# Optimization experiments

Hardware: AMD Instinct MI355X
Metric: run time of the kernel (lower is better)

## Reference

```python
import jax, jax.numpy as jnp
import numpy as np

POLY_Q = 2.0  # normalizer='poly_2'
N_HEADS = 12
LN_EPS = 1e-5  # torch nn.LayerNorm default


def poly_norm(x, q=POLY_Q):
    # Newton solve for c such that sum_k 1/(-x-c)^q == 1, row-wise (last axis).
    c = jnp.min(-x, axis=-1, keepdims=True) - 1.0  # ensures -x - c >= 1
    for _ in range(6):
        base = -x - c
        poly_sum = jnp.sum(base ** (-q), axis=-1, keepdims=True)
        poly_sum_der = q * jnp.sum(base ** (-(q + 1.0)), axis=-1, keepdims=True)
        c = c - (poly_sum - 1.0) / (poly_sum_der + 1e-8)
    return (-x - c) ** (-q)


def layer_norm(x, g, b, eps=LN_EPS):
    m = jnp.mean(x, axis=-1, keepdims=True)
    v = jnp.mean((x - m) ** 2, axis=-1, keepdims=True)
    return (x - m) * jax.lax.rsqrt(v + eps) * g + b


def setup_inputs() -> dict:
    key = jax.random.key(0)
    B, S, D, M = 2, 1024, 768, 3072
    ks = jax.random.split(key, 8)
    sd = 1.0 / np.sqrt(D)
    sm = 1.0 / np.sqrt(M)
    return {
        "x": jax.random.normal(ks[0], (B, S, D), dtype=jnp.float32),
        "ln1_g": jnp.ones((D,), jnp.float32),
        "ln1_b": jnp.zeros((D,), jnp.float32),
        "wq": jax.random.normal(ks[1], (D, D), jnp.float32) * sd,
        "bq": jnp.zeros((D,), jnp.float32),
        "wk": jax.random.normal(ks[2], (D, D), jnp.float32) * sd,
        "bk": jnp.zeros((D,), jnp.float32),
        "wv": jax.random.normal(ks[3], (D, D), jnp.float32) * sd,
        "bv": jnp.zeros((D,), jnp.float32),
        "wo": jax.random.normal(ks[4], (D, D), jnp.float32) * sd,
        "bo": jnp.zeros((D,), jnp.float32),
        "ln2_g": jnp.ones((D,), jnp.float32),
        "ln2_b": jnp.zeros((D,), jnp.float32),
        "w1": jax.random.normal(ks[5], (D, M), jnp.float32) * sd,
        "b1": jnp.zeros((M,), jnp.float32),
        "w2": jax.random.normal(ks[6], (M, D), jnp.float32) * sm,
        "b2": jnp.zeros((D,), jnp.float32),
    }


def reference(x, ln1_g, ln1_b, wq, bq, wk, bk, wv, bv, wo, bo,
              ln2_g, ln2_b, w1, b1, w2, b2):
    B, S, D = x.shape
    H = N_HEADS
    Dh = D // H
    # --- pre-LN self-attention with poly normalizer ---
    y = layer_norm(x, ln1_g, ln1_b)
    q = (y @ wq + bq).reshape(B, S, H, Dh) / jnp.sqrt(jnp.float32(Dh))
    k = (y @ wk + bk).reshape(B, S, H, Dh)
    v = (y @ wv + bv).reshape(B, S, H, Dh)
    scores = jnp.einsum('bqhd,bkhd->bhqk', q, k)  # [B,H,S,S]
    attn_w = poly_norm(scores)
    attn = jnp.einsum('bhqk,bkhd->bqhd', attn_w, v).reshape(B, S, D)
    x1 = x + attn @ wo + bo  # residual 1
    # --- MLP block ---
    y2 = layer_norm(x1, ln2_g, ln2_b)
    h = jax.nn.gelu(y2 @ w1 + b1, approximate=False)  # torch GELU = exact erf
    out = x1 + h @ w2 + b2  # residual 2
    return out
```

## Files before the change

### kernel.cpp

```cpp
#include <hip/hip_runtime.h>

#define DEV __device__ __forceinline__

typedef unsigned short u16;
typedef __attribute__((ext_vector_type(8))) short bf16x8;
typedef __attribute__((ext_vector_type(4))) float f32x4;
typedef __attribute__((ext_vector_type(4))) unsigned int u32x4;

DEV u16 f2bf(float f) {
  union { float f; unsigned u; } un; un.f = f;
  unsigned r = un.u + 0x7fffu + ((un.u >> 16) & 1u);
  return (u16)(r >> 16);
}

DEV void gload16(const void* g, void* l) {
  __builtin_amdgcn_global_load_lds((const __attribute__((address_space(1))) void*)g,
                                   (__attribute__((address_space(3))) void*)l, 16, 0, 0);
}

template <int N>
DEV void vm_wait() { asm volatile("s_waitcnt vmcnt(%0)" :: "n"(N) : "memory"); }

DEV float blk_sum(float v, volatile float* sb) {
#pragma unroll
  for (int o = 32; o; o >>= 1) v += __shfl_xor(v, o);
  __syncthreads();
  if ((threadIdx.x & 63) == 0) sb[threadIdx.x >> 6] = v;
  __syncthreads();
  return sb[0] + sb[1] + sb[2] + sb[3];
}

__global__ __launch_bounds__(256) void ln_kernel(const float* __restrict__ x,
                                                 const float* __restrict__ g,
                                                 const float* __restrict__ b,
                                                 u16* __restrict__ y) {
  __shared__ float sb[4];
  const size_t row = blockIdx.x;
  const float* xr = x + row * 768;
  const int t = threadIdx.x;
  float v0 = xr[t], v1 = xr[t + 256], v2 = xr[t + 512];
  float mean = blk_sum(v0 + v1 + v2, sb) * (1.0f / 768.0f);
  float d0 = v0 - mean, d1 = v1 - mean, d2 = v2 - mean;
  float var = blk_sum(d0 * d0 + d1 * d1 + d2 * d2, sb) * (1.0f / 768.0f);
  float inv = rsqrtf(var + 1e-5f);
  u16* yr = y + row * 768;
  yr[t]       = f2bf(d0 * inv * g[t]       + b[t]);
  yr[t + 256] = f2bf(d1 * inv * g[t + 256] + b[t + 256]);
  yr[t + 512] = f2bf(d2 * inv * g[t + 512] + b[t + 512]);
}

__global__ __launch_bounds__(256) void wt_all(
    const float* __restrict__ wq, const float* __restrict__ wk,
    const float* __restrict__ wv, const float* __restrict__ wo,
    const float* __restrict__ w1, const float* __restrict__ w2,
    u16* __restrict__ oq, u16* __restrict__ ok, u16* __restrict__ ov,
    u16* __restrict__ oo, u16* __restrict__ o1, u16* __restrict__ o2) {
  __shared__ float tile[32][33];
  const int id = blockIdx.x;
  const float* in;
  u16* out;
  int K, N, t, nx;
  if (id < 2304) {
    int s = id / 576;
    t = id % 576;
    K = 768; N = 768; nx = 24;
    in  = (s == 0) ? wq : (s == 1) ? wk : (s == 2) ? wv : wo;
    out = (s == 0) ? oq : (s == 1) ? ok : (s == 2) ? ov : oo;
  } else if (id < 4608) {
    t = id - 2304; in = w1; out = o1; K = 768; N = 3072; nx = 96;
  } else {
    t = id - 4608; in = w2; out = o2; K = 3072; N = 768; nx = 24;
  }
  const int yt = (nx == 96) ? (t / 96) : (t / 24);
  const int xt = t - yt * nx;
  const int n0 = xt * 32, k0 = yt * 32;
  const int tx = threadIdx.x & 31, ty = threadIdx.x >> 5;
#pragma unroll
  for (int i = 0; i < 4; i++)
    tile[ty + 8 * i][tx] = in[(size_t)(k0 + ty + 8 * i) * N + n0 + tx];
  __syncthreads();
#pragma unroll
  for (int i = 0; i < 4; i++)
    out[(size_t)(n0 + ty + 8 * i) * K + k0 + tx] = f2bf(tile[tx][ty + 8 * i]);
}

__global__ __launch_bounds__(512) void fused_attn(const u16* __restrict__ qkv,
                                                  const u16* __restrict__ vT,
                                                  u16* __restrict__ attn) {
  __shared__ __align__(16) u16 wlds[16 * 1024];

  const int tid = threadIdx.x;
  const int w = tid >> 6, l = tid & 63;
  const int g = l >> 4, lr = l & 15;
  const int bh = blockIdx.y, b = bh / 12, h = bh % 12;
  const int q0 = blockIdx.x * 16;

  const u16* qrow = qkv + (size_t)(b * 1024 + q0 + lr) * 2304 + h * 64;
  const u16* krow = qkv + (size_t)(b * 1024 + w * 128 + lr) * 2304 + 768 + h * 64;

  bf16x8 af[2];
  af[0] = *(const bf16x8*)(qrow + g * 8);
  af[1] = *(const bf16x8*)(qrow + 32 + g * 8);

  f32x4 acc[8];
#pragma unroll
  for (int n = 0; n < 8; n++) acc[n] = (f32x4){0.f, 0.f, 0.f, 0.f};

#pragma unroll
  for (int n = 0; n < 8; n++) {
    bf16x8 b0 = *(const bf16x8*)(krow + n * 16 * 2304 + g * 8);
    bf16x8 b1 = *(const bf16x8*)(krow + n * 16 * 2304 + 32 + g * 8);
    acc[n] = __builtin_amdgcn_mfma_f32_16x16x32_bf16(af[0], b0, acc[n], 0, 0, 0);
    acc[n] = __builtin_amdgcn_mfma_f32_16x16x32_bf16(af[1], b1, acc[n], 0, 0, 0);
  }

#pragma unroll
  for (int n = 0; n < 8; n++)
#pragma unroll
    for (int r = 0; r < 4; r++) {
      int row = g * 4 + r;
      int col = w * 128 + n * 16 + lr;
      unsigned off = (unsigned)(row * 2048 + col * 2);
      off ^= (unsigned)(row & 7) << 4;
      *(u16*)((char*)wlds + off) = f2bf(acc[n][r]);
    }
  __syncthreads();

  const int crow = tid >> 5, l32 = tid & 31;
  const unsigned cswz = (unsigned)(crow & 7) << 4;
  const unsigned cbase = (unsigned)(crow * 2048 + l32 * 64);
  float xs[32];
#pragma unroll
  for (int j = 0; j < 4; j++) {
    u32x4 raw = *(const u32x4*)((const char*)wlds + ((cbase + j * 16u) ^ cswz));
#pragma unroll
    for (int e = 0; e < 4; e++) {
      union { unsigned u; float f; } lo, hi;
      lo.u = raw[e] << 16;
      hi.u = raw[e] & 0xffff0000u;
      xs[j * 8 + e * 2] = lo.f;
      xs[j * 8 + e * 2 + 1] = hi.f;
    }
  }

  float mx = xs[0];
#pragma unroll
  for (int i = 1; i < 32; i++) mx = fmaxf(mx, xs[i]);
#pragma unroll
  for (int o = 1; o < 32; o <<= 1) mx = fmaxf(mx, __shfl_xor(mx, o));
  float c = -mx - 1.0f;

#pragma unroll 1
  for (int it = 0; it < 6; it++) {
    float s2 = 0.f, s3 = 0.f;
#pragma unroll
    for (int i = 0; i < 32; i++) {
      float rr = __builtin_amdgcn_rcpf(-(xs[i] + c));
      float r2 = rr * rr;
      s2 += r2;
      s3 = fmaf(r2, rr, s3);
    }
#pragma unroll
    for (int o = 1; o < 32; o <<= 1) {
      s2 += __shfl_xor(s2, o);
      s3 += __shfl_xor(s3, o);
    }
    c -= (s2 - 1.0f) * __builtin_amdgcn_rcpf(2.0f * s3 + 1e-8f);
  }

#pragma unroll
  for (int j = 0; j < 4; j++) {
    u32x4 outv;
#pragma unroll
    for (int e = 0; e < 4; e++) {
      float r0 = __builtin_amdgcn_rcpf(-(xs[j * 8 + e * 2] + c));
      float r1 = __builtin_amdgcn_rcpf(-(xs[j * 8 + e * 2 + 1] + c));
      outv[e] = (unsigned)f2bf(r0 * r0) | ((unsigned)f2bf(r1 * r1) << 16);
    }
    *(u32x4*)((char*)wlds + ((cbase + j * 16u) ^ cswz)) = outv;
  }
  __syncthreads();

  if (w < 4) {
    const int nf = w;
    const u16* vrow = vT + (size_t)(bh * 64 + nf * 16 + lr) * 1024;
    const unsigned swz = (unsigned)(lr & 7) << 4;
    const unsigned abase = (unsigned)(lr * 2048);
    f32x4 oacc = (f32x4){0.f, 0.f, 0.f, 0.f};
#pragma unroll
    for (int ks = 0; ks < 32; ks++) {
      bf16x8 afr = *(const bf16x8*)((const char*)wlds +
                                    ((abase + (unsigned)(ks * 64 + g * 16)) ^ swz));
      bf16x8 bfr = *(const bf16x8*)(vrow + ks * 32 + g * 8);
      oacc = __builtin_amdgcn_mfma_f32_16x16x32_bf16(afr, bfr, oacc, 0, 0, 0);
    }
    u16* orow = attn + (size_t)(b * 1024 + q0 + g * 4) * 768 + h * 64 + nf * 16 + lr;
#pragma unroll
    for (int r = 0; r < 4; r++) orow[(size_t)r * 768] = f2bf(oacc[r]);
  }
}

__global__ __launch_bounds__(256) void splitk_reduce(const float* __restrict__ p,
                                                     const float* __restrict__ bias,
                                                     const float* __restrict__ res,
                                                     float* __restrict__ out) {
  const size_t S = 2048ull * 768;
  size_t i = ((size_t)blockIdx.x * 256 + threadIdx.x) * 4;
  f32x4 v = *(const f32x4*)&p[i];
  v += *(const f32x4*)&p[i + S];
  v += *(const f32x4*)&p[i + 2 * S];
  v += *(const f32x4*)&p[i + 3 * S];
  int col = (int)(i % 768);
  v += *(const f32x4*)&bias[col];
  v += *(const f32x4*)&res[i];
  *(f32x4*)&out[i] = v;
}

template <int BM, int WN, int EPI>
__global__ __launch_bounds__(256) void gemm_bt(
    const u16* __restrict__ A, int lda, long long sAb, long long sAh,
    const u16* __restrict__ B0, const u16* __restrict__ B1, const u16* __restrict__ B2,
    int ldb, long long sBb, long long sBh,
    void* __restrict__ Cv, int ldc, long long sCb, long long sCh,
    const float* __restrict__ bias0, const float* __restrict__ bias1,
    const float* __restrict__ bias2, const float* __restrict__ res, int K) {
  constexpr int WCOL = (BM == 128) ? 2 : 4;
  constexpr int BN = WCOL * WN * 16;
  constexpr int NA = BM / 64;
  constexpr int NB = BN / 64;
  constexpr int LT = NA + NB;
  __shared__ __align__(16) u16 lds_a[3][BM * 32];
  __shared__ __align__(16) u16 lds_b[3][BN * 32];

  const int zb = blockIdx.z / 12, zh = blockIdx.z % 12;
  A += zb * sAb + zh * sAh;

  const int colbase = blockIdx.y * BN;
  const u16* B = B0;
  const float* bias = bias0;
  int biasoff = 0;
  float qscale = 1.0f;
  int sel = 0;
  if (EPI == 0) {
    sel = colbase / 768;
    B = (sel == 0) ? B0 : ((sel == 1) ? B1 : B2);
    bias = (sel == 0) ? bias0 : ((sel == 1) ? bias1 : bias2);
    biasoff = sel * 768;
    qscale = (sel == 0) ? 0.125f : 1.0f;
  }
  B += zb * sBb + zh * sBh;

  const int tid = threadIdx.x;
  const size_t ldab = (size_t)lda * 2, ldbb = (size_t)ldb * 2;
  const char* Abase = (const char*)(A + (size_t)blockIdx.x * BM * lda);
  const char* Bbase = (const char*)(B + (size_t)(colbase - biasoff) * ldb);

  const char* ap[NA];
  const char* bp[NB];
#pragma unroll
  for (int j = 0; j < NA; j++) {
    int lin = (j * 256 + tid) * 16;
    ap[j] = Abase + (size_t)(lin >> 6) * ldab + (lin & 63);
  }
#pragma unroll
  for (int j = 0; j < NB; j++) {
    int lin = (j * 256 + tid) * 16;
    bp[j] = Bbase + (size_t)(lin >> 6) * ldbb + (lin & 63);
  }

  auto stage = [&](int buf) {
#pragma unroll
    for (int j = 0; j < NA; j++) {
      gload16(ap[j], (char*)&lds_a[buf][0] + (j * 256 + tid) * 16);
      ap[j] += 64;
    }
#pragma unroll
    for (int j = 0; j < NB; j++) {
      gload16(bp[j], (char*)&lds_b[buf][0] + (j * 256 + tid) * 16);
      bp[j] += 64;
    }
  };

  f32x4 acc[4][WN];
#pragma unroll
  for (int m = 0; m < 4; m++)
#pragma unroll
    for (int n = 0; n < WN; n++) acc[m][n] = (f32x4){0.f, 0.f, 0.f, 0.f};

  const int w = tid >> 6, l = tid & 63;
  const int wm = (BM == 128) ? (w >> 1) : 0;
  const int wn = (BM == 128) ? (w & 1) : w;
  const int lr = l & 15, kg = l >> 4;

  const int nt = K / 32;
  stage(0);
  if (nt > 1) stage(1);

  for (int t = 0; t < nt; ++t) {
    const int buf = t % 3;
    if (t + 2 < nt) {
      stage((t + 2) % 3);
      vm_wait<2 * LT>();
    } else if (t + 1 < nt) {
      vm_wait<LT>();
    } else {
      vm_wait<0>();
    }
    __builtin_amdgcn_sched_barrier(0);
    __builtin_amdgcn_s_barrier();
    __builtin_amdgcn_sched_barrier(0);

    bf16x8 af[4], bfr[WN];
#pragma unroll
    for (int m = 0; m < 4; m++)
      af[m] = *(const bf16x8*)&lds_a[buf][(wm * 64 + m * 16 + lr) * 32 + kg * 8];
#pragma unroll
    for (int n = 0; n < WN; n++)
      bfr[n] = *(const bf16x8*)&lds_b[buf][(wn * WN * 16 + n * 16 + lr) * 32 + kg * 8];
#pragma unroll
    for (int m = 0; m < 4; m++)
#pragma unroll
      for (int n = 0; n < WN; n++)
        acc[m][n] = __builtin_amdgcn_mfma_f32_16x16x32_bf16(af[m], bfr[n], acc[m][n], 0, 0, 0);

    __builtin_amdgcn_sched_barrier(0);
    __builtin_amdgcn_s_barrier();
    __builtin_amdgcn_sched_barrier(0);
  }

  const int row0 = blockIdx.x * BM + ((BM == 128) ? wm * 64 : 0) + kg * 4;
  const int colb = colbase + wn * WN * 16;
  float* Cf = (float*)Cv + (size_t)zb * sCb + (size_t)zh * sCh;
  u16* Cu = (u16*)Cv + (size_t)zb * sCb + (size_t)zh * sCh;

  if (EPI == 0 && sel == 2) {
    u16* vTp = (u16*)res;
#pragma unroll
    for (int m = 0; m < 4; m++) {
#pragma unroll
      for (int n = 0; n < WN; n++) {
#pragma unroll
        for (int r = 0; r < 4; r++) {
          int row = row0 + m * 16 + r;
          int col = colb + n * 16 + lr;
          int cv = col - 1536;
          int bb = row >> 10, ss = row & 1023;
          int hh = cv >> 6, dd = cv & 63;
          vTp[(size_t)((bb * 12 + hh) * 64 + dd) * 1024 + ss] =
              f2bf(acc[m][n][r] + bias[cv]);
        }
      }
    }
    return;
  }

#pragma unroll
  for (int m = 0; m < 4; m++) {
#pragma unroll
    for (int n = 0; n < WN; n++) {
#pragma unroll
      for (int r = 0; r < 4; r++) {
        int row = row0 + m * 16 + r;
        int col = colb + n * 16 + lr;
        size_t idx = (size_t)row * ldc + col;
        float v = acc[m][n][r];
        if (EPI == 0) {
          Cu[idx] = f2bf((v + bias[col - biasoff]) * qscale);
        } else if (EPI == 1) {
          Cf[idx] = v;
        } else if (EPI == 2) {
          Cu[idx] = f2bf(v);
        } else if (EPI == 3) {
          Cf[idx] = v + bias[col] + res[idx];
        } else {
          v += bias[col];
          Cu[idx] = f2bf(0.5f * v * (1.0f + erff(v * 0.70710678118654752f)));
        }
      }
    }
  }
}

extern "C" void kernel_launch(void* const* d_in, const int* in_sizes, int n_in,
                              void* d_out, int out_size, void* d_ws, size_t ws_size,
                              hipStream_t stream) {
  const float* x     = (const float*)d_in[0];
  const float* ln1_g = (const float*)d_in[1];
  const float* ln1_b = (const float*)d_in[2];
  const float* wq    = (const float*)d_in[3];
  const float* bq    = (const float*)d_in[4];
  const float* wk    = (const float*)d_in[5];
  const float* bk    = (const float*)d_in[6];
  const float* wv    = (const float*)d_in[7];
  const float* bv    = (const float*)d_in[8];
  const float* wo    = (const float*)d_in[9];
  const float* bo    = (const float*)d_in[10];
  const float* ln2_g = (const float*)d_in[11];
  const float* ln2_b = (const float*)d_in[12];
  const float* w1    = (const float*)d_in[13];
  const float* b1    = (const float*)d_in[14];
  const float* w2    = (const float*)d_in[15];
  const float* b2    = (const float*)d_in[16];
  float* out = (float*)d_out;

  char* p = (char*)d_ws;
  auto alloc = [&](size_t n) { char* r = p; p += (n + 255) & ~(size_t)255; return r; };
  u16*   qkv    = (u16*)  alloc(2048ull * 2304 * 2);
  u16*   y1     = (u16*)  alloc(2048ull * 768 * 2);
  u16*   vT     = (u16*)  alloc(24ull * 64 * 1024 * 2);
  u16*   attn   = (u16*)  alloc(2048ull * 768 * 2);
  float* x1     = (float*)alloc(2048ull * 768 * 4);
  u16*   y2     = (u16*)  alloc(2048ull * 768 * 2);
  u16*   hbuf   = (u16*)  alloc(2048ull * 3072 * 2);
  float* pbuf   = (float*)alloc(4ull * 2048 * 768 * 4);
  u16*   wq_t   = (u16*)  alloc(768ull * 768 * 2);
  u16*   wk_t   = (u16*)  alloc(768ull * 768 * 2);
  u16*   wv_t   = (u16*)  alloc(768ull * 768 * 2);
  u16*   wo_t   = (u16*)  alloc(768ull * 768 * 2);
  u16*   w1_t   = (u16*)  alloc(3072ull * 768 * 2);
  u16*   w2_t   = (u16*)  alloc(768ull * 3072 * 2);
  (void)in_sizes; (void)n_in; (void)out_size; (void)ws_size;

  wt_all<<<6912, 256, 0, stream>>>(wq, wk, wv, wo, w1, w2,
                                   wq_t, wk_t, wv_t, wo_t, w1_t, w2_t);

  ln_kernel<<<2048, 256, 0, stream>>>(x, ln1_g, ln1_b, y1);

  gemm_bt<128, 4, 0><<<dim3(16, 18, 1), 256, 0, stream>>>(
      y1, 768, 0, 0, wq_t, wk_t, wv_t, 768, 0, 0, qkv, 2304, 0, 0,
      bq, bk, bv, (const float*)vT, 768);

  fused_attn<<<dim3(64, 24), 512, 0, stream>>>(qkv, vT, attn);

  gemm_bt<64, 2, 3><<<dim3(32, 6, 1), 256, 0, stream>>>(
      attn, 768, 0, 0, wo_t, nullptr, nullptr, 768, 0, 0, x1, 768, 0, 0,
      bo, nullptr, nullptr, x, 768);

  ln_kernel<<<2048, 256, 0, stream>>>(x1, ln2_g, ln2_b, y2);

  gemm_bt<128, 4, 4><<<dim3(16, 24, 1), 256, 0, stream>>>(
      y2, 768, 0, 0, w1_t, nullptr, nullptr, 768, 0, 0, hbuf, 3072, 0, 0,
      b1, nullptr, nullptr, nullptr, 768);

  gemm_bt<64, 2, 1><<<dim3(32, 6, 4), 256, 0, stream>>>(
      hbuf, 3072, 0, 768LL, w2_t, nullptr, nullptr, 3072, 0, 768LL,
      pbuf, 768, 0, 1572864LL, nullptr, nullptr, nullptr, nullptr, 768);

  splitk_reduce<<<1536, 256, 0, stream>>>(pbuf, b2, x1, out);
}
```

Baseline: 170.2 us.

## Pack attention tiles into 1024 blocks and transpose QK MFMA for vectorized stores

Grid of 1536 attention tiles is remapped onto 1024 blocks: half the blocks process two tiles sequentially, half process one, so the grid fits a fixed block count with fewer tail waves. The QK^T MFMA operand order is swapped so each lane holds four consecutive key columns, allowing packed 8-byte LDS stores instead of scalar 2-byte stores. Adds an extra barrier between tiles and uneven per-block work.

```diff
diff --git a/kernel.cpp b/kernel.cpp
--- a/kernel.cpp
+++ b/kernel.cpp
@@ -6,6 +6,7 @@
 typedef __attribute__((ext_vector_type(8))) short bf16x8;
 typedef __attribute__((ext_vector_type(4))) float f32x4;
 typedef __attribute__((ext_vector_type(4))) unsigned int u32x4;
+typedef __attribute__((ext_vector_type(2))) unsigned int u32x2;
 
 DEV u16 f2bf(float f) {
   union { float f; unsigned u; } un; un.f = f;
@@ -92,111 +93,122 @@
   const int tid = threadIdx.x;
   const int w = tid >> 6, l = tid & 63;
   const int g = l >> 4, lr = l & 15;
-  const int bh = blockIdx.y, b = bh / 12, h = bh % 12;
-  const int q0 = blockIdx.x * 16;
-
-  const u16* qrow = qkv + (size_t)(b * 1024 + q0 + lr) * 2304 + h * 64;
-  const u16* krow = qkv + (size_t)(b * 1024 + w * 128 + lr) * 2304 + 768 + h * 64;
-
-  bf16x8 af[2];
-  af[0] = *(const bf16x8*)(qrow + g * 8);
-  af[1] = *(const bf16x8*)(qrow + 32 + g * 8);
-
-  f32x4 acc[8];
-#pragma unroll
-  for (int n = 0; n < 8; n++) acc[n] = (f32x4){0.f, 0.f, 0.f, 0.f};
-
-#pragma unroll
-  for (int n = 0; n < 8; n++) {
-    bf16x8 b0 = *(const bf16x8*)(krow + n * 16 * 2304 + g * 8);
-    bf16x8 b1 = *(const bf16x8*)(krow + n * 16 * 2304 + 32 + g * 8);
-    acc[n] = __builtin_amdgcn_mfma_f32_16x16x32_bf16(af[0], b0, acc[n], 0, 0, 0);
-    acc[n] = __builtin_amdgcn_mfma_f32_16x16x32_bf16(af[1], b1, acc[n], 0, 0, 0);
-  }
-
-#pragma unroll
-  for (int n = 0; n < 8; n++)
-#pragma unroll
-    for (int r = 0; r < 4; r++) {
-      int row = g * 4 + r;
-      int col = w * 128 + n * 16 + lr;
-      unsigned off = (unsigned)(row * 2048 + col * 2);
-      off ^= (unsigned)(row & 7) << 4;
-      *(u16*)((char*)wlds + off) = f2bf(acc[n][r]);
-    }
-  __syncthreads();
-
-  const int crow = tid >> 5, l32 = tid & 31;
-  const unsigned cswz = (unsigned)(crow & 7) << 4;
-  const unsigned cbase = (unsigned)(crow * 2048 + l32 * 64);
-  float xs[32];
-#pragma unroll
-  for (int j = 0; j < 4; j++) {
-    u32x4 raw = *(const u32x4*)((const char*)wlds + ((cbase + j * 16u) ^ cswz));
-#pragma unroll
-    for (int e = 0; e < 4; e++) {
-      union { unsigned u; float f; } lo, hi;
-      lo.u = raw[e] << 16;
-      hi.u = raw[e] & 0xffff0000u;
-      xs[j * 8 + e * 2] = lo.f;
-      xs[j * 8 + e * 2 + 1] = hi.f;
-    }
-  }
-
-  float mx = xs[0];
-#pragma unroll
-  for (int i = 1; i < 32; i++) mx = fmaxf(mx, xs[i]);
-#pragma unroll
-  for (int o = 1; o < 32; o <<= 1) mx = fmaxf(mx, __shfl_xor(mx, o));
-  float c = -mx - 1.0f;
+
+  const int b0 = blockIdx.x;
+  const bool heavy = ((b0 ^ (b0 >> 8)) & 1) == 0;
+  const int ntiles = heavy ? 2 : 1;
+  const int t2 = 1024 + ((b0 >> 8) * 128 + ((b0 & 255) >> 1));
 
 #pragma unroll 1
-  for (int it = 0; it < 6; it++) {
-    float s2 = 0.f, s3 = 0.f;
-#pragma unroll
-    for (int i = 0; i < 32; i++) {
-      float rr = __builtin_amdgcn_rcpf(-(xs[i] + c));
-      float r2 = rr * rr;
-      s2 += r2;
-      s3 = fmaf(r2, rr, s3);
-    }
-#pragma unroll
-    for (int o = 1; o < 32; o <<= 1) {
-      s2 += __shfl_xor(s2, o);
-      s3 += __shfl_xor(s3, o);
-    }
-    c -= (s2 - 1.0f) * __builtin_amdgcn_rcpf(2.0f * s3 + 1e-8f);
-  }
-
-#pragma unroll
-  for (int j = 0; j < 4; j++) {
-    u32x4 outv;
-#pragma unroll
-    for (int e = 0; e < 4; e++) {
-      float r0 = __builtin_amdgcn_rcpf(-(xs[j * 8 + e * 2] + c));
-      float r1 = __builtin_amdgcn_rcpf(-(xs[j * 8 + e * 2 + 1] + c));
-      outv[e] = (unsigned)f2bf(r0 * r0) | ((unsigned)f2bf(r1 * r1) << 16);
-    }
-    *(u32x4*)((char*)wlds + ((cbase + j * 16u) ^ cswz)) = outv;
-  }
-  __syncthreads();
-
-  if (w < 4) {
-    const int nf = w;
-    const u16* vrow = vT + (size_t)(bh * 64 + nf * 16 + lr) * 1024;
-    const unsigned swz = (unsigned)(lr & 7) << 4;
-    const unsigned abase = (unsigned)(lr * 2048);
-    f32x4 oacc = (f32x4){0.f, 0.f, 0.f, 0.f};
-#pragma unroll
-    for (int ks = 0; ks < 32; ks++) {
-      bf16x8 afr = *(const bf16x8*)((const char*)wlds +
-                                    ((abase + (unsigned)(ks * 64 + g * 16)) ^ swz));
-      bf16x8 bfr = *(const bf16x8*)(vrow + ks * 32 + g * 8);
-      oacc = __builtin_amdgcn_mfma_f32_16x16x32_bf16(afr, bfr, oacc, 0, 0, 0);
-    }
-    u16* orow = attn + (size_t)(b * 1024 + q0 + g * 4) * 768 + h * 64 + nf * 16 + lr;
-#pragma unroll
-    for (int r = 0; r < 4; r++) orow[(size_t)r * 768] = f2bf(oacc[r]);
+  for (int it = 0; it < ntiles; ++it) {
+    const int tile = (it == 0) ? b0 : t2;
+    const int bh = tile >> 6, b = bh / 12, h = bh % 12;
+    const int q0 = (tile & 63) * 16;
+
+    const u16* qrow = qkv + (size_t)(b * 1024 + q0 + lr) * 2304 + h * 64;
+    const u16* krow = qkv + (size_t)(b * 1024 + w * 128 + lr) * 2304 + 768 + h * 64;
+
+    bf16x8 qf[2];
+    qf[0] = *(const bf16x8*)(qrow + g * 8);
+    qf[1] = *(const bf16x8*)(qrow + 32 + g * 8);
+
+    f32x4 acc[8];
+#pragma unroll
+    for (int n = 0; n < 8; n++) acc[n] = (f32x4){0.f, 0.f, 0.f, 0.f};
+
+#pragma unroll
+    for (int n = 0; n < 8; n++) {
+      bf16x8 k0 = *(const bf16x8*)(krow + n * 16 * 2304 + g * 8);
+      bf16x8 k1 = *(const bf16x8*)(krow + n * 16 * 2304 + 32 + g * 8);
+      acc[n] = __builtin_amdgcn_mfma_f32_16x16x32_bf16(k0, qf[0], acc[n], 0, 0, 0);
+      acc[n] = __builtin_amdgcn_mfma_f32_16x16x32_bf16(k1, qf[1], acc[n], 0, 0, 0);
+    }
+
+#pragma unroll
+    for (int n = 0; n < 8; n++) {
+      unsigned off = (unsigned)(lr * 2048 + (w * 128 + n * 16 + g * 4) * 2);
+      off ^= (unsigned)(lr & 7) << 4;
+      u32x2 pk;
+      pk[0] = (unsigned)f2bf(acc[n][0]) | ((unsigned)f2bf(acc[n][1]) << 16);
+      pk[1] = (unsigned)f2bf(acc[n][2]) | ((unsigned)f2bf(acc[n][3]) << 16);
+      *(u32x2*)((char*)wlds + off) = pk;
+    }
+    __syncthreads();
+
+    const int crow = tid >> 5, l32 = tid & 31;
+    const unsigned cswz = (unsigned)(crow & 7) << 4;
+    const unsigned cbase = (unsigned)(crow * 2048 + l32 * 64);
+    float xs[32];
+#pragma unroll
+    for (int j = 0; j < 4; j++) {
+      u32x4 raw = *(const u32x4*)((const char*)wlds + ((cbase + j * 16u) ^ cswz));
+#pragma unroll
+      for (int e = 0; e < 4; e++) {
+        union { unsigned u; float f; } lo, hi;
+        lo.u = raw[e] << 16;
+        hi.u = raw[e] & 0xffff0000u;
+        xs[j * 8 + e * 2] = lo.f;
+        xs[j * 8 + e * 2 + 1] = hi.f;
+      }
+    }
+
+    float mx = xs[0];
+#pragma unroll
+    for (int i = 1; i < 32; i++) mx = fmaxf(mx, xs[i]);
+#pragma unroll
+    for (int o = 1; o < 32; o <<= 1) mx = fmaxf(mx, __shfl_xor(mx, o));
+    float c = -mx - 1.0f;
+
+#pragma unroll 1
+    for (int nit = 0; nit < 6; nit++) {
+      float s2 = 0.f, s3 = 0.f;
+#pragma unroll
+      for (int i = 0; i < 32; i++) {
+        float rr = __builtin_amdgcn_rcpf(-(xs[i] + c));
+        float r2 = rr * rr;
+        s2 += r2;
+        s3 = fmaf(r2, rr, s3);
+      }
+#pragma unroll
+      for (int o = 1; o < 32; o <<= 1) {
+        s2 += __shfl_xor(s2, o);
+        s3 += __shfl_xor(s3, o);
+      }
+      c -= (s2 - 1.0f) * __builtin_amdgcn_rcpf(2.0f * s3 + 1e-8f);
+    }
+
+#pragma unroll
+    for (int j = 0; j < 4; j++) {
+      u32x4 outv;
+#pragma unroll
+      for (int e = 0; e < 4; e++) {
+        float r0 = __builtin_amdgcn_rcpf(-(xs[j * 8 + e * 2] + c));
+        float r1 = __builtin_amdgcn_rcpf(-(xs[j * 8 + e * 2 + 1] + c));
+        outv[e] = (unsigned)f2bf(r0 * r0) | ((unsigned)f2bf(r1 * r1) << 16);
+      }
+      *(u32x4*)((char*)wlds + ((cbase + j * 16u) ^ cswz)) = outv;
+    }
+    __syncthreads();
+
+    if (w < 4) {
+      const int nf = w;
+      const u16* vrow = vT + (size_t)(bh * 64 + nf * 16 + lr) * 1024;
+      const unsigned swz = (unsigned)(lr & 7) << 4;
+      const unsigned abase = (unsigned)(lr * 2048);
+      f32x4 oacc = (f32x4){0.f, 0.f, 0.f, 0.f};
+#pragma unroll
+      for (int ks = 0; ks < 32; ks++) {
+        bf16x8 afr = *(const bf16x8*)((const char*)wlds +
+                                      ((abase + (unsigned)(ks * 64 + g * 16)) ^ swz));
+        bf16x8 bfr = *(const bf16x8*)(vrow + ks * 32 + g * 8);
+        oacc = __builtin_amdgcn_mfma_f32_16x16x32_bf16(afr, bfr, oacc, 0, 0, 0);
+      }
+      u16* orow = attn + (size_t)(b * 1024 + q0 + g * 4) * 768 + h * 64 + nf * 16 + lr;
+#pragma unroll
+      for (int r = 0; r < 4; r++) orow[(size_t)r * 768] = f2bf(oacc[r]);
+    }
+
+    if (it + 1 < ntiles) __syncthreads();
   }
 }
 
@@ -430,7 +442,7 @@
       y1, 768, 0, 0, wq_t, wk_t, wv_t, 768, 0, 0, qkv, 2304, 0, 0,
       bq, bk, bv, (const float*)vT, 768);
 
-  fused_attn<<<dim3(64, 24), 512, 0, stream>>>(qkv, vT, attn);
+  fused_attn<<<1024, 512, 0, stream>>>(qkv, vT, attn);
 
   gemm_bt<64, 2, 3><<<dim3(32, 6, 1), 256, 0, stream>>>(
       attn, 768, 0, 0, wo_t, nullptr, nullptr, 768, 0, 0, x1, 768, 0, 0,
```

After: 205.4 us. +20.7%, slower.
